# Kernel tuning notes

Hardware: AMD Instinct MI355X
Metric: run time of the kernel (lower is better)

Reference implementation:

```python
import jax, jax.numpy as jnp
import numpy as np

B, N, H, E = 16, 256, 128, 16
LN_EPS = 1e-5


def setup_inputs() -> dict:
    key = jax.random.key(0)
    ks = jax.random.split(key, 16)
    def lin(k, fan_in, fan_out):
        bound = 1.0 / np.sqrt(fan_in)
        kw, kb = jax.random.split(k)
        W = jax.random.uniform(kw, (fan_in, fan_out), jnp.float32, -bound, bound)
        b = jax.random.uniform(kb, (fan_out,), jnp.float32, -bound, bound)
        return W, b
    dW1, db1 = lin(ks[0], 1, E)
    dW2, db2 = lin(ks[1], E, E)
    uW1, ub1 = lin(ks[2], 2 * H + E, 2 * E)
    uW2, ub2 = lin(ks[3], 2 * E, E)
    nW1, nb1 = lin(ks[4], E, H // 2)
    nW2, nb2 = lin(ks[5], H // 2, H)
    return {
        "node_embeddings": jax.random.normal(ks[6], (B, N, H), jnp.float32),
        "distance_matrix": jax.random.uniform(ks[7], (B, N, N), jnp.float32),
        "visited": jax.random.randint(ks[8], (B, N), 0, 2) > 0,
        "dW1": dW1, "db1": db1, "dW2": dW2, "db2": db2,
        "uW1": uW1, "ub1": ub1,
        "ln_g": jnp.ones((2 * E,), jnp.float32), "ln_b": jnp.zeros((2 * E,), jnp.float32),
        "uW2": uW2, "ub2": ub2,
        "nW1": nW1, "nb1": nb1, "nW2": nW2, "nb2": nb2,
    }


def _layernorm(x, g, b):
    mu = jnp.mean(x, axis=-1, keepdims=True)
    var = jnp.mean((x - mu) ** 2, axis=-1, keepdims=True)
    return (x - mu) * jax.lax.rsqrt(var + LN_EPS) * g + b


def reference(node_embeddings, distance_matrix, visited,
              dW1, db1, dW2, db2,
              uW1, ub1, ln_g, ln_b, uW2, ub2,
              nW1, nb1, nW2, nb2):
    Bn, Nn, Hn = node_embeddings.shape
    # distance encoder: [B,N,N,1] -> [B,N,N,E]
    d = distance_matrix[..., None]
    dist_feat = jax.nn.relu(d @ dW1 + db1) @ dW2 + db2
    # pairwise concat [node_i, node_j, dist] -> edge MLP
    node_i = jnp.broadcast_to(node_embeddings[:, :, None, :], (Bn, Nn, Nn, Hn))
    node_j = jnp.broadcast_to(node_embeddings[:, None, :, :], (Bn, Nn, Nn, Hn))
    edge_input = jnp.concatenate([node_i, node_j, dist_feat], axis=-1)  # [B,N,N,2H+E]
    h = _layernorm(edge_input @ uW1 + ub1, ln_g, ln_b)
    edge_features = jax.nn.relu(h) @ uW2 + ub2  # [B,N,N,E]
    # mask by visited rows (scale by 0.5 where visited)
    scale = 1.0 - visited.astype(edge_features.dtype) * 0.5  # [B,N]
    edge_features = edge_features * scale[:, :, None, None]
    # mean over j, then node MLP
    pooled = jnp.mean(edge_features, axis=2)  # [B,N,E]
    edge_messages = jax.nn.relu(pooled @ nW1 + nb1) @ nW2 + nb2  # [B,N,H]
    return edge_features, edge_messages
```

## Files before the change

### kernel.cpp

```cpp
#include <hip/hip_runtime.h>

#define NB 16
#define NN 256
#define NH 128
#define NE 16

typedef float v4f  __attribute__((ext_vector_type(4)));
typedef short bf16x8 __attribute__((ext_vector_type(8)));
typedef unsigned int uint;

constexpr long long EF_ELEMS = (long long)NB * NN * NN * NE;


__global__ __launch_bounds__(256) void k_prep_proj2(
    const float* __restrict__ node, const float* __restrict__ uW1,
    const float* __restrict__ dW1, const float* __restrict__ db1,
    const float* __restrict__ dW2, const float* __restrict__ db2,
    const float* __restrict__ ub1,
    float* __restrict__ bps, float* __restrict__ albe,
    float* __restrict__ Pi, float* __restrict__ Pj)
{
    const int t = threadIdx.x;
    if (blockIdx.x == 2048) {
        __shared__ float sM[512];
        __shared__ float sBp[16];
        __shared__ float sA[16], sB[16];
        for (int i = t; i < 512; i += 256) {
            const int k = i >> 5, c = i & 31;
            float s = 0.f;
#pragma unroll
            for (int e = 0; e < 16; ++e)
                s = fmaf(dW2[k * 16 + e], uW1[(256 + e) * 32 + c], s);
            sM[i] = s;
        }
        if (t < 16) { sA[t] = dW1[t]; sB[t] = db1[t]; }
        __syncthreads();
        if (t < 16) {
            const float a = sA[t];
            const float x = (a != 0.f) ? (-sB[t] / a) : -1e30f;
            int r = 0;
            for (int q = 0; q < 16; ++q) {
                const float aq = sA[q];
                const float xq = (aq != 0.f) ? (-sB[q] / aq) : -1e30f;
                r += (xq < x) || (xq == x && q < t);
            }
            sBp[r] = x;
        }
        __syncthreads();
        if (t < 16) bps[t] = sBp[t];
        for (int i = t; i < 544; i += 256) {
            const int s = i >> 5, c = i & 31;
            float dt;
            if (s == 0)       dt = sBp[0] - 1.0f;
            else if (s == 16) dt = sBp[15] + 1.0f;
            else              dt = 0.5f * (sBp[s - 1] + sBp[s]);
            float alpha = 0.f, beta = 0.f;
#pragma unroll
            for (int k = 0; k < 16; ++k) {
                if (fmaf(sA[k], dt, sB[k]) > 0.f) {
                    const float m = sM[k * 32 + c];
                    alpha = fmaf(sA[k], m, alpha);
                    beta  = fmaf(sB[k], m, beta);
                }
            }
            float c2 = ub1[c];
#pragma unroll
            for (int e = 0; e < 16; ++e)
                c2 = fmaf(db2[e], uW1[(256 + e) * 32 + c], c2);
            albe[s * 68 + c]      = alpha;
            albe[s * 68 + 32 + c] = beta + c2;
        }
        for (int i = 1156 + t; i < 1280; i += 256) albe[i] = 0.f;
    } else {
        const int r    = t >> 7;
        const int half = (t >> 6) & 1;
        const int ks   = (t >> 5) & 1;
        const int c    = t & 31;
        const int row  = blockIdx.x * 2 + r;
        __shared__ float nrow[2][128];
        nrow[r][t & 127] = node[(size_t)row * 128 + (t & 127)];
        __syncthreads();
        const float* w = uW1 + half * 128 * 32 + c;
        const int k0 = ks * 64;
        float s = 0.f;
#pragma unroll 8
        for (int k = 0; k < 64; ++k)
            s = fmaf(nrow[r][k0 + k], w[(size_t)(k0 + k) * 32], s);
        s += __shfl_xor(s, 32);
        if (!(t & 32))
            (half ? Pj : Pi)[(size_t)row * 32 + c] = s;
    }
}

__global__ __launch_bounds__(256) void k_edge7(
    const float* __restrict__ dist, const int* __restrict__ visited,
    const float* __restrict__ ln_g, const float* __restrict__ ln_b,
    const float* __restrict__ uW2, const float* __restrict__ ub2,
    const float* __restrict__ bps, const float* __restrict__ albe_g,
    const float* __restrict__ Pi, const float* __restrict__ Pj,
    const float* __restrict__ nW1, const float* __restrict__ nb1,
    const float* __restrict__ nW2, const float* __restrict__ nb2,
    float* __restrict__ ef_out, float* __restrict__ msg_out)
{
    const int row0 = blockIdx.x * 4;
    const int b = row0 >> 8;
    const int j = threadIdx.x;

    __shared__ float albe_s[1280];
    __shared__ uint  h_lds[256 * 20];
    __shared__ float Pi_s[4][32];
    __shared__ float red2[4][4][16];
    __shared__ float pool_s[4][16];
    __shared__ float hid_s[4][64];

    {
        const float4* ag = reinterpret_cast<const float4*>(albe_g);
        float4* as = reinterpret_cast<float4*>(albe_s);
        for (int q = j; q < 320; q += 256) as[q] = ag[q];
    }
    if (j < 128) Pi_s[j >> 5][j & 31] = Pi[(size_t)row0 * 32 + j];

    float scv[4];
#pragma unroll
    for (int r = 0; r < 4; ++r) scv[r] = visited[row0 + r] ? 0.5f : 1.0f;

    const int lane = j & 63, wv = j >> 6;
    const int eRow = lane & 15;
    const int g    = lane >> 4;

    bf16x8 ahi, alo;
    {
        union { uint u[4]; bf16x8 v; } Uhi, Ulo;
#pragma unroll
        for (int p = 0; p < 4; ++p) {
            const int q = g * 4 + p;
            const float w0 = uW2[(2 * q) * 16 + eRow];
            const float w1 = uW2[(2 * q + 1) * 16 + eRow];
            uint W00, W11, Whi, Wlo;
            asm("v_cvt_pk_bf16_f32 %0, %1, %2" : "=v"(W00) : "v"(w0), "v"(w0));
            asm("v_cvt_pk_bf16_f32 %0, %1, %2" : "=v"(W11) : "v"(w1), "v"(w1));
            const float w0h = __uint_as_float(W00 << 16);
            const float w1h = __uint_as_float(W11 << 16);
            asm("v_cvt_pk_bf16_f32 %0, %1, %2" : "=v"(Whi) : "v"(w0), "v"(w1));
            asm("v_cvt_pk_bf16_f32 %0, %1, %2" : "=v"(Wlo) : "v"(w0 - w0h), "v"(w1 - w1h));
            Uhi.u[p] = Whi;
            Ulo.u[p] = Wlo;
        }
        ahi = Uhi.v;
        alo = Ulo.v;
    }

    float dq[4];
#pragma unroll
    for (int r = 0; r < 4; ++r)
        dq[r] = dist[(size_t)(row0 + r) * NN + j];

    const float4 ub2v = *reinterpret_cast<const float4*>(&ub2[g * 4]);
    const float4* pj4 = reinterpret_cast<const float4*>(Pj + ((size_t)(b * NN + j)) * 32);
    float4 pj[8];
#pragma unroll
    for (int q = 0; q < 8; ++q) pj[q] = pj4[q];

    __syncthreads();

#pragma unroll
    for (int r = 0; r < 4; ++r) {
        const int row = row0 + r;
        const float d = dq[r];

        int seg = 0;
#pragma unroll
        for (int k = 0; k < 16; ++k) seg += (d > bps[k]) ? 1 : 0;
        const float* ab = &albe_s[seg * 68];

        float pre[32];
#pragma unroll
        for (int q = 0; q < 8; ++q) {
            const v4f piv = *reinterpret_cast<const v4f*>(&Pi_s[r][q * 4]);
            const float4 al = *reinterpret_cast<const float4*>(&ab[q * 4]);
            const float4 be = *reinterpret_cast<const float4*>(&ab[32 + q * 4]);
            pre[q * 4 + 0] = piv.x + pj[q].x + fmaf(d, al.x, be.x);
            pre[q * 4 + 1] = piv.y + pj[q].y + fmaf(d, al.y, be.y);
            pre[q * 4 + 2] = piv.z + pj[q].z + fmaf(d, al.z, be.z);
            pre[q * 4 + 3] = piv.w + pj[q].w + fmaf(d, al.w, be.w);
        }

        float s0 = 0.f, s1 = 0.f, s2 = 0.f, s3 = 0.f;
#pragma unroll
        for (int c = 0; c < 32; c += 4) { s0 += pre[c]; s1 += pre[c+1]; s2 += pre[c+2]; s3 += pre[c+3]; }
        const float mu = ((s0 + s1) + (s2 + s3)) * (1.f / 32.f);
        float v0 = 0.f, v1 = 0.f, v2 = 0.f, v3 = 0.f;
#pragma unroll
        for (int c = 0; c < 32; c += 4) {
            pre[c]   -= mu; v0 = fmaf(pre[c],   pre[c],   v0);
            pre[c+1] -= mu; v1 = fmaf(pre[c+1], pre[c+1], v1);
            pre[c+2] -= mu; v2 = fmaf(pre[c+2], pre[c+2], v2);
            pre[c+3] -= mu; v3 = fmaf(pre[c+3], pre[c+3], v3);
        }
        const float rstd = rsqrtf(fmaf((v0 + v1) + (v2 + v3), 1.f / 32.f, 1e-5f));

#pragma unroll
        for (int c = 0; c < 32; ++c)
            pre[c] = fmaxf(fmaf(pre[c] * rstd, ln_g[c], ln_b[c]), 0.f);
        {
            uint hw[16];
#pragma unroll
            for (int q = 0; q < 16; ++q) {
                uint rr;
                asm("v_cvt_pk_bf16_f32 %0, %1, %2" : "=v"(rr) : "v"(pre[2*q]), "v"(pre[2*q+1]));
                hw[q] = rr;
            }
            uint* hrow = &h_lds[j * 20];
            *reinterpret_cast<uint4*>(hrow + 0)  = make_uint4(hw[0],  hw[1],  hw[2],  hw[3]);
            *reinterpret_cast<uint4*>(hrow + 4)  = make_uint4(hw[4],  hw[5],  hw[6],  hw[7]);
            *reinterpret_cast<uint4*>(hrow + 8)  = make_uint4(hw[8],  hw[9],  hw[10], hw[11]);
            *reinterpret_cast<uint4*>(hrow + 12) = make_uint4(hw[12], hw[13], hw[14], hw[15]);
        }

        const float scale = scv[r];
        v4f accsum = {0.f, 0.f, 0.f, 0.f};
#pragma unroll
        for (int t = 0; t < 4; ++t) {
            const int edge = wv * 64 + t * 16 + eRow;
            const bf16x8 bfr = *reinterpret_cast<const bf16x8*>(&h_lds[edge * 20 + g * 4]);
            v4f acc = {ub2v.x, ub2v.y, ub2v.z, ub2v.w};
            acc = __builtin_amdgcn_mfma_f32_16x16x32_bf16(alo, bfr, acc, 0, 0, 0);
            acc = __builtin_amdgcn_mfma_f32_16x16x32_bf16(ahi, bfr, acc, 0, 0, 0);
            acc[0] *= scale; acc[1] *= scale; acc[2] *= scale; acc[3] *= scale;
            *reinterpret_cast<v4f*>(ef_out + ((size_t)row * NN + edge) * 16 + g * 4) = acc;
            accsum += acc;
        }
#pragma unroll
        for (int rr = 0; rr < 4; ++rr) {
            float v = accsum[rr];
            v += __shfl_xor(v, 1);
            v += __shfl_xor(v, 2);
            v += __shfl_xor(v, 4);
            v += __shfl_xor(v, 8);
            accsum[rr] = v;
        }
        if (eRow == 0)
            *reinterpret_cast<v4f*>(&red2[r][wv][g * 4]) = accsum;
    }

    __syncthreads();

    if (j < 64) {
        const int r = j >> 4, e = j & 15;
        pool_s[r][e] = (red2[r][0][e] + red2[r][1][e] + red2[r][2][e] + red2[r][3][e])
                       * (1.f / 256.f);
    }
    __syncthreads();

    {
        const int r = j >> 6, u = j & 63;
        float s = nb1[u];
#pragma unroll
        for (int e = 0; e < 16; ++e)
            s = fmaf(pool_s[r][e], nW1[e * 64 + u], s);
        hid_s[r][u] = fmaxf(s, 0.f);
    }
    __syncthreads();

#pragma unroll
    for (int p = 0; p < 2; ++p) {
        const int idx = p * 256 + j;
        const int r = idx >> 7, o = idx & 127;
        float s = nb2[o];
#pragma unroll 8
        for (int q = 0; q < 64; ++q)
            s = fmaf(hid_s[r][q], nW2[q * 128 + o], s);
        msg_out[(size_t)(row0 + r) * 128 + o] = s;
    }
}

extern "C" void kernel_launch(void* const* d_in, const int* in_sizes, int n_in,
                              void* d_out, int out_size, void* d_ws, size_t ws_size,
                              hipStream_t stream)
{
    const float* node    = (const float*)d_in[0];
    const float* dist    = (const float*)d_in[1];
    const int*   visited = (const int*)  d_in[2];
    const float* dW1     = (const float*)d_in[3];
    const float* db1     = (const float*)d_in[4];
    const float* dW2     = (const float*)d_in[5];
    const float* db2     = (const float*)d_in[6];
    const float* uW1     = (const float*)d_in[7];
    const float* ub1     = (const float*)d_in[8];
    const float* ln_g    = (const float*)d_in[9];
    const float* ln_b    = (const float*)d_in[10];
    const float* uW2     = (const float*)d_in[11];
    const float* ub2     = (const float*)d_in[12];
    const float* nW1     = (const float*)d_in[13];
    const float* nb1     = (const float*)d_in[14];
    const float* nW2     = (const float*)d_in[15];
    const float* nb2     = (const float*)d_in[16];

    float* ws   = (float*)d_ws;
    float* bps  = ws;
    float* albe = ws + 16;
    float* Pi   = ws + 16 + 1280;
    float* Pj   = Pi + 4096 * 32;

    float* out = (float*)d_out;
    float* msg = out + EF_ELEMS;

    hipLaunchKernelGGL(k_prep_proj2, dim3(2049), dim3(256), 0, stream,
                       node, uW1, dW1, db1, dW2, db2, ub1, bps, albe, Pi, Pj);
    hipLaunchKernelGGL(k_edge7, dim3(1024), dim3(256), 0, stream,
                       dist, visited, ln_g, ln_b, uW2, ub2, bps, albe, Pi, Pj,
                       nW1, nb1, nW2, nb2, out, msg);
}
```

Before: 42.93 us.

## Distribute LayerNorm across MFMA lane groups and halve rows per block

```diff
diff --git a/kernel.cpp b/kernel.cpp
--- a/kernel.cpp
+++ b/kernel.cpp
@@ -92,7 +92,7 @@
     }
 }
 
-__global__ __launch_bounds__(256) void k_edge7(
+__global__ __launch_bounds__(256) void k_edge8(
     const float* __restrict__ dist, const int* __restrict__ visited,
     const float* __restrict__ ln_g, const float* __restrict__ ln_b,
     const float* __restrict__ uW2, const float* __restrict__ ub2,
@@ -102,31 +102,36 @@
     const float* __restrict__ nW2, const float* __restrict__ nb2,
     float* __restrict__ ef_out, float* __restrict__ msg_out)
 {
-    const int row0 = blockIdx.x * 4;
+    const int row0 = blockIdx.x * 2;
     const int b = row0 >> 8;
     const int j = threadIdx.x;
 
     __shared__ float albe_s[1280];
-    __shared__ uint  h_lds[256 * 20];
-    __shared__ float Pi_s[4][32];
-    __shared__ float red2[4][4][16];
-    __shared__ float pool_s[4][16];
-    __shared__ float hid_s[4][64];
+    __shared__ float red2[2][4][16];
+    __shared__ float pool_s[2][16];
+    __shared__ float hid_s[2][64];
 
     {
         const float4* ag = reinterpret_cast<const float4*>(albe_g);
         float4* as = reinterpret_cast<float4*>(albe_s);
         for (int q = j; q < 320; q += 256) as[q] = ag[q];
     }
-    if (j < 128) Pi_s[j >> 5][j & 31] = Pi[(size_t)row0 * 32 + j];
-
-    float scv[4];
-#pragma unroll
-    for (int r = 0; r < 4; ++r) scv[r] = visited[row0 + r] ? 0.5f : 1.0f;
 
     const int lane = j & 63, wv = j >> 6;
     const int eRow = lane & 15;
     const int g    = lane >> 4;
+
+    float gl[8], bl[8];
+    {
+        const float4 g0 = *reinterpret_cast<const float4*>(&ln_g[g * 8]);
+        const float4 g1 = *reinterpret_cast<const float4*>(&ln_g[g * 8 + 4]);
+        const float4 b0 = *reinterpret_cast<const float4*>(&ln_b[g * 8]);
+        const float4 b1 = *reinterpret_cast<const float4*>(&ln_b[g * 8 + 4]);
+        gl[0]=g0.x; gl[1]=g0.y; gl[2]=g0.z; gl[3]=g0.w;
+        gl[4]=g1.x; gl[5]=g1.y; gl[6]=g1.z; gl[7]=g1.w;
+        bl[0]=b0.x; bl[1]=b0.y; bl[2]=b0.z; bl[3]=b0.w;
+        bl[4]=b1.x; bl[5]=b1.y; bl[6]=b1.z; bl[7]=b1.w;
+    }
 
     bf16x8 ahi, alo;
     {
@@ -150,86 +155,92 @@
         alo = Ulo.v;
     }
 
-    float dq[4];
-#pragma unroll
-    for (int r = 0; r < 4; ++r)
+    float dq[2];
+    int   sq[2];
+#pragma unroll
+    for (int r = 0; r < 2; ++r) {
         dq[r] = dist[(size_t)(row0 + r) * NN + j];
+        int seg = 0;
+#pragma unroll
+        for (int k = 0; k < 16; ++k) seg += (dq[r] > bps[k]) ? 1 : 0;
+        sq[r] = seg;
+    }
+
+    float scv[2];
+#pragma unroll
+    for (int r = 0; r < 2; ++r) scv[r] = visited[row0 + r] ? 0.5f : 1.0f;
 
     const float4 ub2v = *reinterpret_cast<const float4*>(&ub2[g * 4]);
-    const float4* pj4 = reinterpret_cast<const float4*>(Pj + ((size_t)(b * NN + j)) * 32);
-    float4 pj[8];
-#pragma unroll
-    for (int q = 0; q < 8; ++q) pj[q] = pj4[q];
 
     __syncthreads();
 
 #pragma unroll
-    for (int r = 0; r < 4; ++r) {
+    for (int r = 0; r < 2; ++r) {
         const int row = row0 + r;
-        const float d = dq[r];
-
-        int seg = 0;
-#pragma unroll
-        for (int k = 0; k < 16; ++k) seg += (d > bps[k]) ? 1 : 0;
-        const float* ab = &albe_s[seg * 68];
-
-        float pre[32];
-#pragma unroll
-        for (int q = 0; q < 8; ++q) {
-            const v4f piv = *reinterpret_cast<const v4f*>(&Pi_s[r][q * 4]);
-            const float4 al = *reinterpret_cast<const float4*>(&ab[q * 4]);
-            const float4 be = *reinterpret_cast<const float4*>(&ab[32 + q * 4]);
-            pre[q * 4 + 0] = piv.x + pj[q].x + fmaf(d, al.x, be.x);
-            pre[q * 4 + 1] = piv.y + pj[q].y + fmaf(d, al.y, be.y);
-            pre[q * 4 + 2] = piv.z + pj[q].z + fmaf(d, al.z, be.z);
-            pre[q * 4 + 3] = piv.w + pj[q].w + fmaf(d, al.w, be.w);
-        }
-
-        float s0 = 0.f, s1 = 0.f, s2 = 0.f, s3 = 0.f;
-#pragma unroll
-        for (int c = 0; c < 32; c += 4) { s0 += pre[c]; s1 += pre[c+1]; s2 += pre[c+2]; s3 += pre[c+3]; }
-        const float mu = ((s0 + s1) + (s2 + s3)) * (1.f / 32.f);
-        float v0 = 0.f, v1 = 0.f, v2 = 0.f, v3 = 0.f;
-#pragma unroll
-        for (int c = 0; c < 32; c += 4) {
-            pre[c]   -= mu; v0 = fmaf(pre[c],   pre[c],   v0);
-            pre[c+1] -= mu; v1 = fmaf(pre[c+1], pre[c+1], v1);
-            pre[c+2] -= mu; v2 = fmaf(pre[c+2], pre[c+2], v2);
-            pre[c+3] -= mu; v3 = fmaf(pre[c+3], pre[c+3], v3);
-        }
-        const float rstd = rsqrtf(fmaf((v0 + v1) + (v2 + v3), 1.f / 32.f, 1e-5f));
-
-#pragma unroll
-        for (int c = 0; c < 32; ++c)
-            pre[c] = fmaxf(fmaf(pre[c] * rstd, ln_g[c], ln_b[c]), 0.f);
-        {
-            uint hw[16];
-#pragma unroll
-            for (int q = 0; q < 16; ++q) {
+        const float scale = scv[r];
+
+        const float4 pi0 = *reinterpret_cast<const float4*>(Pi + (size_t)row * 32 + g * 8);
+        const float4 pi1 = *reinterpret_cast<const float4*>(Pi + (size_t)row * 32 + g * 8 + 4);
+        const float piv[8] = {pi0.x, pi0.y, pi0.z, pi0.w, pi1.x, pi1.y, pi1.z, pi1.w};
+
+        v4f accsum = {0.f, 0.f, 0.f, 0.f};
+#pragma unroll
+        for (int p = 0; p < 4; ++p) {
+            const int edge = wv * 64 + p * 16 + eRow;
+
+            const float dsw = __shfl(dq[r], p * 16 + eRow);
+            const int   ssw = __shfl(sq[r], p * 16 + eRow);
+
+            const float* ab = &albe_s[ssw * 68 + g * 8];
+            const float4 al0 = *reinterpret_cast<const float4*>(&ab[0]);
+            const float4 al1 = *reinterpret_cast<const float4*>(&ab[4]);
+            const float4 be0 = *reinterpret_cast<const float4*>(&ab[32]);
+            const float4 be1 = *reinterpret_cast<const float4*>(&ab[36]);
+
+            const float* pjp = Pj + ((size_t)(b * NN) + edge) * 32 + g * 8;
+            const float4 pj0 = *reinterpret_cast<const float4*>(pjp);
+            const float4 pj1 = *reinterpret_cast<const float4*>(pjp + 4);
+
+            float pre[8];
+            pre[0] = piv[0] + pj0.x + fmaf(dsw, al0.x, be0.x);
+            pre[1] = piv[1] + pj0.y + fmaf(dsw, al0.y, be0.y);
+            pre[2] = piv[2] + pj0.z + fmaf(dsw, al0.z, be0.z);
+            pre[3] = piv[3] + pj0.w + fmaf(dsw, al0.w, be0.w);
+            pre[4] = piv[4] + pj1.x + fmaf(dsw, al1.x, be1.x);
+            pre[5] = piv[5] + pj1.y + fmaf(dsw, al1.y, be1.y);
+            pre[6] = piv[6] + pj1.z + fmaf(dsw, al1.z, be1.z);
+            pre[7] = piv[7] + pj1.w + fmaf(dsw, al1.w, be1.w);
+
+            float s  = ((pre[0] + pre[1]) + (pre[2] + pre[3]))
+                     + ((pre[4] + pre[5]) + (pre[6] + pre[7]));
+            float qq = fmaf(pre[0], pre[0], fmaf(pre[1], pre[1],
+                       fmaf(pre[2], pre[2], pre[3] * pre[3])))
+                     + fmaf(pre[4], pre[4], fmaf(pre[5], pre[5],
+                       fmaf(pre[6], pre[6], pre[7] * pre[7])));
+            s  += __shfl_xor(s, 16);  s  += __shfl_xor(s, 32);
+            qq += __shfl_xor(qq, 16); qq += __shfl_xor(qq, 32);
+            const float mu   = s * (1.f / 32.f);
+            const float var  = fmaf(-mu, mu, qq * (1.f / 32.f));
+            const float rstd = rsqrtf(fmaxf(var, 0.f) + 1e-5f);
+
+            union { uint u[4]; bf16x8 v; } Bf;
+#pragma unroll
+            for (int m = 0; m < 4; ++m) {
+                const float h0 = fmaxf(fmaf((pre[2*m]   - mu) * rstd, gl[2*m],   bl[2*m]),   0.f);
+                const float h1 = fmaxf(fmaf((pre[2*m+1] - mu) * rstd, gl[2*m+1], bl[2*m+1]), 0.f);
                 uint rr;
-                asm("v_cvt_pk_bf16_f32 %0, %1, %2" : "=v"(rr) : "v"(pre[2*q]), "v"(pre[2*q+1]));
-                hw[q] = rr;
+                asm("v_cvt_pk_bf16_f32 %0, %1, %2" : "=v"(rr) : "v"(h0), "v"(h1));
+                Bf.u[m] = rr;
             }
-            uint* hrow = &h_lds[j * 20];
-            *reinterpret_cast<uint4*>(hrow + 0)  = make_uint4(hw[0],  hw[1],  hw[2],  hw[3]);
-            *reinterpret_cast<uint4*>(hrow + 4)  = make_uint4(hw[4],  hw[5],  hw[6],  hw[7]);
-            *reinterpret_cast<uint4*>(hrow + 8)  = make_uint4(hw[8],  hw[9],  hw[10], hw[11]);
-            *reinterpret_cast<uint4*>(hrow + 12) = make_uint4(hw[12], hw[13], hw[14], hw[15]);
-        }
-
-        const float scale = scv[r];
-        v4f accsum = {0.f, 0.f, 0.f, 0.f};
-#pragma unroll
-        for (int t = 0; t < 4; ++t) {
-            const int edge = wv * 64 + t * 16 + eRow;
-            const bf16x8 bfr = *reinterpret_cast<const bf16x8*>(&h_lds[edge * 20 + g * 4]);
+
             v4f acc = {ub2v.x, ub2v.y, ub2v.z, ub2v.w};
-            acc = __builtin_amdgcn_mfma_f32_16x16x32_bf16(alo, bfr, acc, 0, 0, 0);
-            acc = __builtin_amdgcn_mfma_f32_16x16x32_bf16(ahi, bfr, acc, 0, 0, 0);
+            acc = __builtin_amdgcn_mfma_f32_16x16x32_bf16(alo, Bf.v, acc, 0, 0, 0);
+            acc = __builtin_amdgcn_mfma_f32_16x16x32_bf16(ahi, Bf.v, acc, 0, 0, 0);
             acc[0] *= scale; acc[1] *= scale; acc[2] *= scale; acc[3] *= scale;
             *reinterpret_cast<v4f*>(ef_out + ((size_t)row * NN + edge) * 16 + g * 4) = acc;
             accsum += acc;
         }
+
 #pragma unroll
         for (int rr = 0; rr < 4; ++rr) {
             float v = accsum[rr];
@@ -245,14 +256,14 @@
 
     __syncthreads();
 
-    if (j < 64) {
+    if (j < 32) {
         const int r = j >> 4, e = j & 15;
         pool_s[r][e] = (red2[r][0][e] + red2[r][1][e] + red2[r][2][e] + red2[r][3][e])
                        * (1.f / 256.f);
     }
     __syncthreads();
 
-    {
+    if (j < 128) {
         const int r = j >> 6, u = j & 63;
         float s = nb1[u];
 #pragma unroll
@@ -262,10 +273,8 @@
     }
     __syncthreads();
 
-#pragma unroll
-    for (int p = 0; p < 2; ++p) {
-        const int idx = p * 256 + j;
-        const int r = idx >> 7, o = idx & 127;
+    {
+        const int r = j >> 7, o = j & 127;
         float s = nb2[o];
 #pragma unroll 8
         for (int q = 0; q < 64; ++q)
@@ -307,7 +316,7 @@
 
     hipLaunchKernelGGL(k_prep_proj2, dim3(2049), dim3(256), 0, stream,
                        node, uW1, dW1, db1, dW2, db2, ub1, bps, albe, Pi, Pj);
-    hipLaunchKernelGGL(k_edge7, dim3(1024), dim3(256), 0, stream,
+    hipLaunchKernelGGL(k_edge8, dim3(2048), dim3(256), 0, stream,
                        dist, visited, ln_g, ln_b, uW2, ub2, bps, albe, Pi, Pj,
                        nW1, nb1, nW2, nb2, out, msg);
 }
```

Measured after the change: 46.18 us. 7.6% more time.

## Compute distance encoder and edge MLP with 32x32 MFMA instead of piecewise table

Applied to the files above, without the earlier changes.

```diff
diff --git a/kernel.cpp b/kernel.cpp
--- a/kernel.cpp
+++ b/kernel.cpp
@@ -5,26 +5,48 @@
 #define NH 128
 #define NE 16
 
-typedef float v4f  __attribute__((ext_vector_type(4)));
+typedef float v4f    __attribute__((ext_vector_type(4)));
+typedef float f32x16 __attribute__((ext_vector_type(16)));
 typedef short bf16x8 __attribute__((ext_vector_type(8)));
 typedef unsigned int uint;
 
 constexpr long long EF_ELEMS = (long long)NB * NN * NN * NE;
 
 
-__global__ __launch_bounds__(256) void k_prep_proj2(
+__device__ __forceinline__ void pk_hilo(float x0, float x1, uint& hi, uint& lo) {
+    uint h;
+    asm("v_cvt_pk_bf16_f32 %0, %1, %2" : "=v"(h) : "v"(x0), "v"(x1));
+    const float h0 = __uint_as_float(h << 16);
+    const float h1 = __uint_as_float(h & 0xFFFF0000u);
+    uint l;
+    asm("v_cvt_pk_bf16_f32 %0, %1, %2" : "=v"(l) : "v"(x0 - h0), "v"(x1 - h1));
+    hi = h; lo = l;
+}
+
+template <int CTRL>
+__device__ __forceinline__ float dpp_add(float x) {
+    int y = __builtin_amdgcn_update_dpp(0, __float_as_int(x), CTRL, 0xF, 0xF, true);
+    return x + __int_as_float(y);
+}
+__device__ __forceinline__ float halfsum32(float v) {
+    v = dpp_add<0xB1>(v);
+    v = dpp_add<0x4E>(v);
+    v = dpp_add<0x124>(v);
+    v = dpp_add<0x128>(v);
+    v += __shfl_xor(v, 16);
+    return v;
+}
+
+__global__ __launch_bounds__(256) void k_prep_proj3(
     const float* __restrict__ node, const float* __restrict__ uW1,
-    const float* __restrict__ dW1, const float* __restrict__ db1,
     const float* __restrict__ dW2, const float* __restrict__ db2,
     const float* __restrict__ ub1,
-    float* __restrict__ bps, float* __restrict__ albe,
+    float* __restrict__ Mt, float* __restrict__ c2,
     float* __restrict__ Pi, float* __restrict__ Pj)
 {
     const int t = threadIdx.x;
     if (blockIdx.x == 2048) {
         __shared__ float sM[512];
-        __shared__ float sBp[16];
-        __shared__ float sA[16], sB[16];
         for (int i = t; i < 512; i += 256) {
             const int k = i >> 5, c = i & 31;
             float s = 0.f;
@@ -33,44 +55,16 @@
                 s = fmaf(dW2[k * 16 + e], uW1[(256 + e) * 32 + c], s);
             sM[i] = s;
         }
-        if (t < 16) { sA[t] = dW1[t]; sB[t] = db1[t]; }
         __syncthreads();
-        if (t < 16) {
-            const float a = sA[t];
-            const float x = (a != 0.f) ? (-sB[t] / a) : -1e30f;
-            int r = 0;
-            for (int q = 0; q < 16; ++q) {
-                const float aq = sA[q];
-                const float xq = (aq != 0.f) ? (-sB[q] / aq) : -1e30f;
-                r += (xq < x) || (xq == x && q < t);
-            }
-            sBp[r] = x;
-        }
-        __syncthreads();
-        if (t < 16) bps[t] = sBp[t];
-        for (int i = t; i < 544; i += 256) {
-            const int s = i >> 5, c = i & 31;
-            float dt;
-            if (s == 0)       dt = sBp[0] - 1.0f;
-            else if (s == 16) dt = sBp[15] + 1.0f;
-            else              dt = 0.5f * (sBp[s - 1] + sBp[s]);
-            float alpha = 0.f, beta = 0.f;
-#pragma unroll
-            for (int k = 0; k < 16; ++k) {
-                if (fmaf(sA[k], dt, sB[k]) > 0.f) {
-                    const float m = sM[k * 32 + c];
-                    alpha = fmaf(sA[k], m, alpha);
-                    beta  = fmaf(sB[k], m, beta);
-                }
-            }
-            float c2 = ub1[c];
+        for (int i = t; i < 512; i += 256)
+            Mt[(i & 31) * 16 + (i >> 5)] = sM[i];
+        if (t < 32) {
+            float s2 = ub1[t];
 #pragma unroll
             for (int e = 0; e < 16; ++e)
-                c2 = fmaf(db2[e], uW1[(256 + e) * 32 + c], c2);
-            albe[s * 68 + c]      = alpha;
-            albe[s * 68 + 32 + c] = beta + c2;
-        }
-        for (int i = 1156 + t; i < 1280; i += 256) albe[i] = 0.f;
+                s2 = fmaf(db2[e], uW1[(256 + e) * 32 + t], s2);
+            c2[t] = s2;
+        }
     } else {
         const int r    = t >> 7;
         const int half = (t >> 6) & 1;
@@ -92,11 +86,12 @@
     }
 }
 
-__global__ __launch_bounds__(256) void k_edge7(
+__global__ __launch_bounds__(256) void k_edge11(
     const float* __restrict__ dist, const int* __restrict__ visited,
     const float* __restrict__ ln_g, const float* __restrict__ ln_b,
     const float* __restrict__ uW2, const float* __restrict__ ub2,
-    const float* __restrict__ bps, const float* __restrict__ albe_g,
+    const float* __restrict__ dW1, const float* __restrict__ db1,
+    const float* __restrict__ Mt, const float* __restrict__ c2g,
     const float* __restrict__ Pi, const float* __restrict__ Pj,
     const float* __restrict__ nW1, const float* __restrict__ nb1,
     const float* __restrict__ nW2, const float* __restrict__ nb2,
@@ -106,141 +101,172 @@
     const int b = row0 >> 8;
     const int j = threadIdx.x;
 
-    __shared__ float albe_s[1280];
-    __shared__ uint  h_lds[256 * 20];
-    __shared__ float Pi_s[4][32];
     __shared__ float red2[4][4][16];
     __shared__ float pool_s[4][16];
     __shared__ float hid_s[4][64];
 
-    {
-        const float4* ag = reinterpret_cast<const float4*>(albe_g);
-        float4* as = reinterpret_cast<float4*>(albe_s);
-        for (int q = j; q < 320; q += 256) as[q] = ag[q];
-    }
-    if (j < 128) Pi_s[j >> 5][j & 31] = Pi[(size_t)row0 * 32 + j];
+    const int lane = j & 63, wv = j >> 6;
+    const int e32 = lane & 31;
+    const int s   = lane >> 5;
+
+    bf16x8 Mth, Mtl;
+    {
+        union { uint u[4]; bf16x8 v; } H, L;
+        const float4 mA = *reinterpret_cast<const float4*>(Mt + e32 * 16 + 8 * s);
+        const float4 mB = *reinterpret_cast<const float4*>(Mt + e32 * 16 + 8 * s + 4);
+        const float mv[8] = {mA.x, mA.y, mA.z, mA.w, mB.x, mB.y, mB.z, mB.w};
+#pragma unroll
+        for (int i = 0; i < 4; ++i) pk_hilo(mv[2 * i], mv[2 * i + 1], H.u[i], L.u[i]);
+        Mth = H.v; Mtl = L.v;
+    }
+    bf16x8 A0h, A0l, A1h, A1l;
+    {
+#pragma unroll
+        for (int Hh = 0; Hh < 2; ++Hh) {
+            union { uint u[4]; bf16x8 v; } H, L;
+            const int base = 16 * Hh + 4 * s;
+            const int cpr[8] = {base, base + 1, base + 2, base + 3,
+                                base + 8, base + 9, base + 10, base + 11};
+            float w[8];
+#pragma unroll
+            for (int i = 0; i < 8; ++i)
+                w[i] = (e32 < 16) ? uW2[cpr[i] * 16 + e32] : 0.f;
+#pragma unroll
+            for (int i = 0; i < 4; ++i) pk_hilo(w[2 * i], w[2 * i + 1], H.u[i], L.u[i]);
+            if (Hh == 0) { A0h = H.v; A0l = L.v; } else { A1h = H.v; A1l = L.v; }
+        }
+    }
+    float aK[8], bK[8];
+    {
+        const float4 aA = *reinterpret_cast<const float4*>(dW1 + 8 * s);
+        const float4 aB = *reinterpret_cast<const float4*>(dW1 + 8 * s + 4);
+        const float4 bA = *reinterpret_cast<const float4*>(db1 + 8 * s);
+        const float4 bB = *reinterpret_cast<const float4*>(db1 + 8 * s + 4);
+        aK[0]=aA.x; aK[1]=aA.y; aK[2]=aA.z; aK[3]=aA.w;
+        aK[4]=aB.x; aK[5]=aB.y; aK[6]=aB.z; aK[7]=aB.w;
+        bK[0]=bA.x; bK[1]=bA.y; bK[2]=bA.z; bK[3]=bA.w;
+        bK[4]=bB.x; bK[5]=bB.y; bK[6]=bB.z; bK[7]=bB.w;
+    }
+    f32x16 ub2i;
+    {
+        const float4 uA = *reinterpret_cast<const float4*>(ub2 + 4 * s);
+        const float4 uB = *reinterpret_cast<const float4*>(ub2 + 8 + 4 * s);
+        ub2i[0]=uA.x; ub2i[1]=uA.y; ub2i[2]=uA.z; ub2i[3]=uA.w;
+        ub2i[4]=uB.x; ub2i[5]=uB.y; ub2i[6]=uB.z; ub2i[7]=uB.w;
+#pragma unroll
+        for (int m = 8; m < 16; ++m) ub2i[m] = 0.f;
+    }
+    float gl[16], bl[16];
+#pragma unroll
+    for (int q = 0; q < 4; ++q) {
+        const int off = q * 8 + 4 * s;
+        const float4 gv = *reinterpret_cast<const float4*>(ln_g + off);
+        const float4 bv = *reinterpret_cast<const float4*>(ln_b + off);
+        gl[q*4+0]=gv.x; gl[q*4+1]=gv.y; gl[q*4+2]=gv.z; gl[q*4+3]=gv.w;
+        bl[q*4+0]=bv.x; bl[q*4+1]=bv.y; bl[q*4+2]=bv.z; bl[q*4+3]=bv.w;
+    }
 
     float scv[4];
 #pragma unroll
     for (int r = 0; r < 4; ++r) scv[r] = visited[row0 + r] ? 0.5f : 1.0f;
 
-    const int lane = j & 63, wv = j >> 6;
-    const int eRow = lane & 15;
-    const int g    = lane >> 4;
-
-    bf16x8 ahi, alo;
-    {
-        union { uint u[4]; bf16x8 v; } Uhi, Ulo;
-#pragma unroll
-        for (int p = 0; p < 4; ++p) {
-            const int q = g * 4 + p;
-            const float w0 = uW2[(2 * q) * 16 + eRow];
-            const float w1 = uW2[(2 * q + 1) * 16 + eRow];
-            uint W00, W11, Whi, Wlo;
-            asm("v_cvt_pk_bf16_f32 %0, %1, %2" : "=v"(W00) : "v"(w0), "v"(w0));
-            asm("v_cvt_pk_bf16_f32 %0, %1, %2" : "=v"(W11) : "v"(w1), "v"(w1));
-            const float w0h = __uint_as_float(W00 << 16);
-            const float w1h = __uint_as_float(W11 << 16);
-            asm("v_cvt_pk_bf16_f32 %0, %1, %2" : "=v"(Whi) : "v"(w0), "v"(w1));
-            asm("v_cvt_pk_bf16_f32 %0, %1, %2" : "=v"(Wlo) : "v"(w0 - w0h), "v"(w1 - w1h));
-            Uhi.u[p] = Whi;
-            Ulo.u[p] = Wlo;
-        }
-        ahi = Uhi.v;
-        alo = Ulo.v;
-    }
-
-    float dq[4];
-#pragma unroll
-    for (int r = 0; r < 4; ++r)
-        dq[r] = dist[(size_t)(row0 + r) * NN + j];
-
-    const float4 ub2v = *reinterpret_cast<const float4*>(&ub2[g * 4]);
-    const float4* pj4 = reinterpret_cast<const float4*>(Pj + ((size_t)(b * NN + j)) * 32);
-    float4 pj[8];
-#pragma unroll
-    for (int q = 0; q < 8; ++q) pj[q] = pj4[q];
-
-    __syncthreads();
-
-#pragma unroll
     for (int r = 0; r < 4; ++r) {
         const int row = row0 + r;
-        const float d = dq[r];
-
-        int seg = 0;
-#pragma unroll
-        for (int k = 0; k < 16; ++k) seg += (d > bps[k]) ? 1 : 0;
-        const float* ab = &albe_s[seg * 68];
-
-        float pre[32];
-#pragma unroll
-        for (int q = 0; q < 8; ++q) {
-            const v4f piv = *reinterpret_cast<const v4f*>(&Pi_s[r][q * 4]);
-            const float4 al = *reinterpret_cast<const float4*>(&ab[q * 4]);
-            const float4 be = *reinterpret_cast<const float4*>(&ab[32 + q * 4]);
-            pre[q * 4 + 0] = piv.x + pj[q].x + fmaf(d, al.x, be.x);
-            pre[q * 4 + 1] = piv.y + pj[q].y + fmaf(d, al.y, be.y);
-            pre[q * 4 + 2] = piv.z + pj[q].z + fmaf(d, al.z, be.z);
-            pre[q * 4 + 3] = piv.w + pj[q].w + fmaf(d, al.w, be.w);
-        }
-
-        float s0 = 0.f, s1 = 0.f, s2 = 0.f, s3 = 0.f;
-#pragma unroll
-        for (int c = 0; c < 32; c += 4) { s0 += pre[c]; s1 += pre[c+1]; s2 += pre[c+2]; s3 += pre[c+3]; }
-        const float mu = ((s0 + s1) + (s2 + s3)) * (1.f / 32.f);
-        float v0 = 0.f, v1 = 0.f, v2 = 0.f, v3 = 0.f;
-#pragma unroll
-        for (int c = 0; c < 32; c += 4) {
-            pre[c]   -= mu; v0 = fmaf(pre[c],   pre[c],   v0);
-            pre[c+1] -= mu; v1 = fmaf(pre[c+1], pre[c+1], v1);
-            pre[c+2] -= mu; v2 = fmaf(pre[c+2], pre[c+2], v2);
-            pre[c+3] -= mu; v3 = fmaf(pre[c+3], pre[c+3], v3);
-        }
-        const float rstd = rsqrtf(fmaf((v0 + v1) + (v2 + v3), 1.f / 32.f, 1e-5f));
-
-#pragma unroll
-        for (int c = 0; c < 32; ++c)
-            pre[c] = fmaxf(fmaf(pre[c] * rstd, ln_g[c], ln_b[c]), 0.f);
-        {
-            uint hw[16];
-#pragma unroll
-            for (int q = 0; q < 16; ++q) {
+        const float scale = scv[r];
+
+        f32x16 cin;
+#pragma unroll
+        for (int q = 0; q < 4; ++q) {
+            const int off = q * 8 + 4 * s;
+            const float4 pv = *reinterpret_cast<const float4*>(Pi + (size_t)row * 32 + off);
+            const float4 cv = *reinterpret_cast<const float4*>(c2g + off);
+            cin[q*4+0] = pv.x + cv.x; cin[q*4+1] = pv.y + cv.y;
+            cin[q*4+2] = pv.z + cv.z; cin[q*4+3] = pv.w + cv.w;
+        }
+
+        float accsum[8];
+#pragma unroll
+        for (int m = 0; m < 8; ++m) accsum[m] = 0.f;
+
+#pragma unroll
+        for (int p = 0; p < 2; ++p) {
+            const int edge = wv * 64 + p * 32 + e32;
+            const float d = dist[(size_t)row * NN + edge];
+
+            bf16x8 Th, Tl;
+            {
+                union { uint u[4]; bf16x8 v; } H, L;
+                float tv[8];
+#pragma unroll
+                for (int i = 0; i < 8; ++i)
+                    tv[i] = fmaxf(fmaf(aK[i], d, bK[i]), 0.f);
+#pragma unroll
+                for (int i = 0; i < 4; ++i) pk_hilo(tv[2*i], tv[2*i+1], H.u[i], L.u[i]);
+                Th = H.v; Tl = L.v;
+            }
+
+            f32x16 acc = __builtin_amdgcn_mfma_f32_32x32x16_bf16(Mth, Th, cin, 0, 0, 0);
+            acc = __builtin_amdgcn_mfma_f32_32x32x16_bf16(Mtl, Th, acc, 0, 0, 0);
+            acc = __builtin_amdgcn_mfma_f32_32x32x16_bf16(Mth, Tl, acc, 0, 0, 0);
+
+            const float* pjp = Pj + ((size_t)(b * NN) + edge) * 32;
+            float pre[16];
+#pragma unroll
+            for (int q = 0; q < 4; ++q) {
+                const int off = q * 8 + 4 * s;
+                const float4 pv = *reinterpret_cast<const float4*>(pjp + off);
+                pre[q*4+0] = acc[q*4+0] + pv.x; pre[q*4+1] = acc[q*4+1] + pv.y;
+                pre[q*4+2] = acc[q*4+2] + pv.z; pre[q*4+3] = acc[q*4+3] + pv.w;
+            }
+
+            float s1 = 0.f, qq = 0.f;
+#pragma unroll
+            for (int m = 0; m < 16; ++m) { s1 += pre[m]; qq = fmaf(pre[m], pre[m], qq); }
+            s1 += __shfl_xor(s1, 32);
+            qq += __shfl_xor(qq, 32);
+            const float mu   = s1 * (1.f / 32.f);
+            const float var  = fmaf(-mu, mu, qq * (1.f / 32.f));
+            const float rstd = rsqrtf(fmaxf(var, 0.f) + 1e-5f);
+
+            float h[16];
+#pragma unroll
+            for (int m = 0; m < 16; ++m)
+                h[m] = fmaxf(fmaf((pre[m] - mu) * rstd, gl[m], bl[m]), 0.f);
+
+            union { uint u[4]; bf16x8 v; } B0, B1;
+#pragma unroll
+            for (int i = 0; i < 4; ++i) {
                 uint rr;
-                asm("v_cvt_pk_bf16_f32 %0, %1, %2" : "=v"(rr) : "v"(pre[2*q]), "v"(pre[2*q+1]));
-                hw[q] = rr;
+                asm("v_cvt_pk_bf16_f32 %0, %1, %2" : "=v"(rr) : "v"(h[2*i]), "v"(h[2*i+1]));
+                B0.u[i] = rr;
             }
-            uint* hrow = &h_lds[j * 20];
-            *reinterpret_cast<uint4*>(hrow + 0)  = make_uint4(hw[0],  hw[1],  hw[2],  hw[3]);
-            *reinterpret_cast<uint4*>(hrow + 4)  = make_uint4(hw[4],  hw[5],  hw[6],  hw[7]);
-            *reinterpret_cast<uint4*>(hrow + 8)  = make_uint4(hw[8],  hw[9],  hw[10], hw[11]);
-            *reinterpret_cast<uint4*>(hrow + 12) = make_uint4(hw[12], hw[13], hw[14], hw[15]);
-        }
-
-        const float scale = scv[r];
-        v4f accsum = {0.f, 0.f, 0.f, 0.f};
-#pragma unroll
-        for (int t = 0; t < 4; ++t) {
-            const int edge = wv * 64 + t * 16 + eRow;
-            const bf16x8 bfr = *reinterpret_cast<const bf16x8*>(&h_lds[edge * 20 + g * 4]);
-            v4f acc = {ub2v.x, ub2v.y, ub2v.z, ub2v.w};
-            acc = __builtin_amdgcn_mfma_f32_16x16x32_bf16(alo, bfr, acc, 0, 0, 0);
-            acc = __builtin_amdgcn_mfma_f32_16x16x32_bf16(ahi, bfr, acc, 0, 0, 0);
-            acc[0] *= scale; acc[1] *= scale; acc[2] *= scale; acc[3] *= scale;
-            *reinterpret_cast<v4f*>(ef_out + ((size_t)row * NN + edge) * 16 + g * 4) = acc;
-            accsum += acc;
-        }
-#pragma unroll
-        for (int rr = 0; rr < 4; ++rr) {
-            float v = accsum[rr];
-            v += __shfl_xor(v, 1);
-            v += __shfl_xor(v, 2);
-            v += __shfl_xor(v, 4);
-            v += __shfl_xor(v, 8);
-            accsum[rr] = v;
-        }
-        if (eRow == 0)
-            *reinterpret_cast<v4f*>(&red2[r][wv][g * 4]) = accsum;
+#pragma unroll
+            for (int i = 0; i < 4; ++i) {
+                uint rr;
+                asm("v_cvt_pk_bf16_f32 %0, %1, %2" : "=v"(rr) : "v"(h[8+2*i]), "v"(h[8+2*i+1]));
+                B1.u[i] = rr;
+            }
+
+            f32x16 ef = __builtin_amdgcn_mfma_f32_32x32x16_bf16(A0h, B0.v, ub2i, 0, 0, 0);
+            ef = __builtin_amdgcn_mfma_f32_32x32x16_bf16(A0l, B0.v, ef, 0, 0, 0);
+            ef = __builtin_amdgcn_mfma_f32_32x32x16_bf16(A1h, B1.v, ef, 0, 0, 0);
+            ef = __builtin_amdgcn_mfma_f32_32x32x16_bf16(A1l, B1.v, ef, 0, 0, 0);
+
+            const float e0 = ef[0]*scale, e1 = ef[1]*scale, e2 = ef[2]*scale, e3 = ef[3]*scale;
+            const float e4 = ef[4]*scale, e5 = ef[5]*scale, e6 = ef[6]*scale, e7 = ef[7]*scale;
+            float* op = ef_out + ((size_t)row * NN + edge) * 16;
+            *reinterpret_cast<v4f*>(op + 4 * s)     = (v4f){e0, e1, e2, e3};
+            *reinterpret_cast<v4f*>(op + 8 + 4 * s) = (v4f){e4, e5, e6, e7};
+            accsum[0] += e0; accsum[1] += e1; accsum[2] += e2; accsum[3] += e3;
+            accsum[4] += e4; accsum[5] += e5; accsum[6] += e6; accsum[7] += e7;
+        }
+
+#pragma unroll
+        for (int m = 0; m < 8; ++m) accsum[m] = halfsum32(accsum[m]);
+        if (e32 == 0) {
+            *reinterpret_cast<v4f*>(&red2[r][wv][4 * s])     = (v4f){accsum[0], accsum[1], accsum[2], accsum[3]};
+            *reinterpret_cast<v4f*>(&red2[r][wv][8 + 4 * s]) = (v4f){accsum[4], accsum[5], accsum[6], accsum[7]};
+        }
     }
 
     __syncthreads();
@@ -254,11 +280,11 @@
 
     {
         const int r = j >> 6, u = j & 63;
-        float s = nb1[u];
+        float sum = nb1[u];
 #pragma unroll
         for (int e = 0; e < 16; ++e)
-            s = fmaf(pool_s[r][e], nW1[e * 64 + u], s);
-        hid_s[r][u] = fmaxf(s, 0.f);
+            sum = fmaf(pool_s[r][e], nW1[e * 64 + u], sum);
+        hid_s[r][u] = fmaxf(sum, 0.f);
     }
     __syncthreads();
 
@@ -266,11 +292,11 @@
     for (int p = 0; p < 2; ++p) {
         const int idx = p * 256 + j;
         const int r = idx >> 7, o = idx & 127;
-        float s = nb2[o];
+        float sum = nb2[o];
 #pragma unroll 8
         for (int q = 0; q < 64; ++q)
-            s = fmaf(hid_s[r][q], nW2[q * 128 + o], s);
-        msg_out[(size_t)(row0 + r) * 128 + o] = s;
+            sum = fmaf(hid_s[r][q], nW2[q * 128 + o], sum);
+        msg_out[(size_t)(row0 + r) * 128 + o] = sum;
     }
 }
 
@@ -297,17 +323,17 @@
     const float* nb2     = (const float*)d_in[16];
 
     float* ws   = (float*)d_ws;
-    float* bps  = ws;
-    float* albe = ws + 16;
-    float* Pi   = ws + 16 + 1280;
+    float* Mt   = ws;
+    float* c2   = ws + 512;
+    float* Pi   = ws + 544;
     float* Pj   = Pi + 4096 * 32;
 
     float* out = (float*)d_out;
     float* msg = out + EF_ELEMS;
 
-    hipLaunchKernelGGL(k_prep_proj2, dim3(2049), dim3(256), 0, stream,
-                       node, uW1, dW1, db1, dW2, db2, ub1, bps, albe, Pi, Pj);
-    hipLaunchKernelGGL(k_edge7, dim3(1024), dim3(256), 0, stream,
-                       dist, visited, ln_g, ln_b, uW2, ub2, bps, albe, Pi, Pj,
+    hipLaunchKernelGGL(k_prep_proj3, dim3(2049), dim3(256), 0, stream,
+                       node, uW1, dW2, db2, ub1, Mt, c2, Pi, Pj);
+    hipLaunchKernelGGL(k_edge11, dim3(1024), dim3(256), 0, stream,
+                       dist, visited, ln_g, ln_b, uW2, ub2, dW1, db1, Mt, c2, Pi, Pj,
                        nW1, nb1, nW2, nb2, out, msg);
 }
```

Result: slower. 48.72 us (+13.5%).
